# Kernel optimization log

Hardware: AMD Instinct MI355X
Metric: run time of the kernel (lower is better)

Reference implementation:

```python
import jax, jax.numpy as jnp
import numpy as np

B = 2048          # batch_size from init
D = 512           # embedding dim
TAU = 0.5         # temperature
EPS = 1e-12       # torch F.normalize eps


def _l2_normalize(x):
    n = jnp.linalg.norm(x, axis=1, keepdims=True)
    return x / jnp.maximum(n, EPS)


def setup_inputs() -> dict:
    key = jax.random.key(0)
    k1, k2 = jax.random.split(key)
    emb_i = jax.random.normal(k1, (2 * B, D), dtype=jnp.float32)
    emb_j = jax.random.normal(k2, (2 * B, D), dtype=jnp.float32)
    return {"emb_i": emb_i, "emb_j": emb_j}


def reference(emb_i, emb_j):
    z_i = _l2_normalize(emb_i)
    z_j = _l2_normalize(emb_j)
    rep = jnp.concatenate([z_i, z_j], axis=0)        # [4B, D], unit rows
    # cosine similarity of unit vectors == plain GEMM
    sim = rep @ rep.T                                # [4B, 4B]
    n = 4 * B
    pos1 = jnp.concatenate([jnp.diagonal(sim, B), jnp.diagonal(sim, -B)])        # [6B]
    pos2 = jnp.concatenate([jnp.diagonal(sim, 2 * B), jnp.diagonal(sim, -2 * B)])  # [4B]
    pos3 = jnp.concatenate([jnp.diagonal(sim, 3 * B), jnp.diagonal(sim, -3 * B)])  # [2B]
    nominator = (jnp.sum(jnp.exp(pos1 / TAU))
                 + jnp.sum(jnp.exp(pos2 / TAU))
                 + jnp.sum(jnp.exp(pos3 / TAU)))
    off_diag = 1.0 - jnp.eye(n, dtype=sim.dtype)
    denominator = jnp.sum(off_diag * jnp.exp(sim / TAU)) - nominator
    loss = -jnp.log(nominator / denominator) / (4 * B)
    return loss
```

## Files before the change

kernel.cpp:

```cpp
#include <hip/hip_runtime.h>
#include <stdint.h>

#define DIM       512
#define NROWS     8192
#define HALF_ROWS 4096
#define TILE      128
#define BK        32

typedef float  floatx4 __attribute__((ext_vector_type(4)));
typedef __bf16 bf16x8  __attribute__((ext_vector_type(8)));

__device__ __forceinline__ void async_copy16(const unsigned short* g, unsigned short* l) {
    __builtin_amdgcn_global_load_lds(
        (const __attribute__((address_space(1))) uint32_t*)(g),
        (__attribute__((address_space(3))) uint32_t*)(l),
        16, 0, 0);
}

__global__ void init_ws(double* ws) {
    ws[0] = 0.0;
    ws[1] = 0.0;
}

__global__ __launch_bounds__(256) void normalize_kernel(
    const float* __restrict__ emb_i, const float* __restrict__ emb_j,
    unsigned short* __restrict__ rep)
{
    const int wave = threadIdx.x >> 6;
    const int lane = threadIdx.x & 63;
    const int row  = blockIdx.x * 4 + wave;
    const float* src = (row < HALF_ROWS) ? (emb_i + (size_t)row * DIM)
                                         : (emb_j + (size_t)(row - HALF_ROWS) * DIM);
    const int c = lane * 8;
    float4 v0 = *(const float4*)(src + c);
    float4 v1 = *(const float4*)(src + c + 4);
    float s = v0.x*v0.x + v0.y*v0.y + v0.z*v0.z + v0.w*v0.w
            + v1.x*v1.x + v1.y*v1.y + v1.z*v1.z + v1.w*v1.w;
    #pragma unroll
    for (int off = 32; off; off >>= 1) s += __shfl_xor(s, off, 64);
    const float nrm = sqrtf(s);
    const float inv = 1.0f / fmaxf(nrm, 1e-12f);
    float f[8] = {v0.x*inv, v0.y*inv, v0.z*inv, v0.w*inv,
                  v1.x*inv, v1.y*inv, v1.z*inv, v1.w*inv};
    union { unsigned short h[8]; uint4 u; } pk;
    #pragma unroll
    for (int t = 0; t < 8; ++t) {
        uint32_t b = __float_as_uint(f[t]);
        b += 0x7FFFu + ((b >> 16) & 1u);
        pk.h[t] = (unsigned short)(b >> 16);
    }
    *(uint4*)(rep + (size_t)row * DIM + c) = pk.u;
}

__global__ __launch_bounds__(256) void gram_kernel(
    const unsigned short* __restrict__ rep, double* __restrict__ ws)
{
    const int bj = blockIdx.x, bi = blockIdx.y;
    if (bj < bi) return;

    __shared__ unsigned short As[TILE * BK];
    __shared__ unsigned short Bs[TILE * BK];
    __shared__ float red[8];

    const int tid  = threadIdx.x;
    const int wave = tid >> 6, lane = tid & 63;
    const int wm = wave >> 1, wn = wave & 1;
    const int m = lane & 15, quad = lane >> 4;

    floatx4 acc[4][4];
    #pragma unroll
    for (int a = 0; a < 4; ++a)
        #pragma unroll
        for (int b = 0; b < 4; ++b)
            #pragma unroll
            for (int e = 0; e < 4; ++e) acc[a][b][e] = 0.0f;

    const int i0 = bi * TILE, j0 = bj * TILE;

    for (int k0 = 0; k0 < DIM; k0 += BK) {
        #pragma unroll
        for (int r = 0; r < 2; ++r) {
            const int chunk = r * 256 + tid;
            const int row   = chunk >> 2;
            const int cc    = (chunk & 3) * 8;
            async_copy16(rep + (size_t)(i0 + row) * DIM + k0 + cc, As + chunk * 8);
            async_copy16(rep + (size_t)(j0 + row) * DIM + k0 + cc, Bs + chunk * 8);
        }
        __syncthreads();

        bf16x8 af[4], bfr[4];
        #pragma unroll
        for (int mt = 0; mt < 4; ++mt)
            af[mt] = *(const bf16x8*)(As + (wm * 64 + mt * 16 + m) * BK + quad * 8);
        #pragma unroll
        for (int nt = 0; nt < 4; ++nt)
            bfr[nt] = *(const bf16x8*)(Bs + (wn * 64 + nt * 16 + m) * BK + quad * 8);
        #pragma unroll
        for (int mt = 0; mt < 4; ++mt)
            #pragma unroll
            for (int nt = 0; nt < 4; ++nt)
                acc[mt][nt] = __builtin_amdgcn_mfma_f32_16x16x32_bf16(
                    af[mt], bfr[nt], acc[mt][nt], 0, 0, 0);
        __syncthreads();
    }

    float s_all = 0.0f, s_pos = 0.0f;
    const float LOG2E2 = 2.885390081777927f;
    #pragma unroll
    for (int mt = 0; mt < 4; ++mt) {
        const int ibase = i0 + wm * 64 + mt * 16 + quad * 4;
        #pragma unroll
        for (int nt = 0; nt < 4; ++nt) {
            const int j = j0 + wn * 64 + nt * 16 + m;
            const floatx4 a = acc[mt][nt];
            #pragma unroll
            for (int r2 = 0; r2 < 4; ++r2) {
                const int i = ibase + r2;
                const float e = exp2f(a[r2] * LOG2E2);
                if (i != j) s_all += e;
                const int d = j - i;
                if (d == 2048 || d == 4096 || d == 6144) s_pos += e;
            }
        }
    }
    #pragma unroll
    for (int off = 32; off; off >>= 1) {
        s_all += __shfl_xor(s_all, off, 64);
        s_pos += __shfl_xor(s_pos, off, 64);
    }
    if (lane == 0) { red[wave] = s_all; red[4 + wave] = s_pos; }
    __syncthreads();
    if (tid == 0) {
        const float w  = (bi == bj) ? 1.0f : 2.0f;
        const float ta = (red[0] + red[1] + red[2] + red[3]) * w;
        const float tp = (red[4] + red[5] + red[6] + red[7]) * w;
        atomicAdd(&ws[0], (double)ta);
        atomicAdd(&ws[1], (double)tp);
    }
}

__global__ void finalize_kernel(const double* __restrict__ ws, float* __restrict__ out) {
    const double nom = ws[1];
    const double den = ws[0] - nom;
    out[0] = (float)(-log(nom / den) / (double)NROWS);
}

extern "C" void kernel_launch(void* const* d_in, const int* in_sizes, int n_in,
                              void* d_out, int out_size, void* d_ws, size_t ws_size,
                              hipStream_t stream) {
    const float* emb_i = (const float*)d_in[0];
    const float* emb_j = (const float*)d_in[1];
    float* out = (float*)d_out;
    double* ws = (double*)d_ws;
    unsigned short* rep = (unsigned short*)((char*)d_ws + 256);

    hipLaunchKernelGGL(init_ws, dim3(1), dim3(1), 0, stream, ws);
    hipLaunchKernelGGL(normalize_kernel, dim3(NROWS / 4), dim3(256), 0, stream,
                       emb_i, emb_j, rep);
    hipLaunchKernelGGL(gram_kernel, dim3(64, 64), dim3(256), 0, stream, rep, ws);
    hipLaunchKernelGGL(finalize_kernel, dim3(1), dim3(1), 0, stream, ws, out);
}
```

Measured before the change: 147.8 us.

## Rewrite gram kernel as 256x256 triangular-tiled, swizzled, double-buffered MFMA pipeline

The gram kernel now uses 256x256 tiles with 8 waves. It launches only the 528 upper-triangle tiles instead of a 64x64 grid with early exits. K-slices of 64 are staged into XOR-swizzled LDS with asynchronous global-to-LDS copies, double-buffered and interleaved with MFMA phases under explicit barriers and priority hints. The init kernel is folded into the normalize kernel to save a launch. This is meant to raise MFMA utilisation and hide load latency, at the cost of more LDS (128KB per block), higher register pressure and a hand-tuned schedule that depends on vmcnt counts being exactly right.

New measurement: 136.4 us. 1.08x faster.

```diff
diff --git a/kernel.cpp b/kernel.cpp
--- a/kernel.cpp
+++ b/kernel.cpp
@@ -1,11 +1,12 @@
 #include <hip/hip_runtime.h>
 #include <stdint.h>
+#include <math.h>
 
 #define DIM       512
 #define NROWS     8192
 #define HALF_ROWS 4096
-#define TILE      128
-#define BK        32
+#define NT        32
+#define NTRI      528
 
 typedef float  floatx4 __attribute__((ext_vector_type(4)));
 typedef __bf16 bf16x8  __attribute__((ext_vector_type(8)));
@@ -17,15 +18,11 @@
         16, 0, 0);
 }
 
-__global__ void init_ws(double* ws) {
-    ws[0] = 0.0;
-    ws[1] = 0.0;
-}
-
 __global__ __launch_bounds__(256) void normalize_kernel(
     const float* __restrict__ emb_i, const float* __restrict__ emb_j,
-    unsigned short* __restrict__ rep)
+    unsigned short* __restrict__ rep, double* __restrict__ ws)
 {
+    if (blockIdx.x == 0 && threadIdx.x == 0) { ws[0] = 0.0; ws[1] = 0.0; }
     const int wave = threadIdx.x >> 6;
     const int lane = threadIdx.x & 63;
     const int row  = blockIdx.x * 4 + wave;
@@ -52,74 +49,155 @@
     *(uint4*)(rep + (size_t)row * DIM + c) = pk.u;
 }
 
-__global__ __launch_bounds__(256) void gram_kernel(
+__device__ __forceinline__ void stage_half(const unsigned short* __restrict__ rep,
+    int rowbase, int k0, unsigned short* lds, int tid)
+{
+    #pragma unroll
+    for (int l = 0; l < 2; ++l) {
+        const int ch  = l * 512 + tid;
+        const int row = ch >> 3;
+        const int s   = ch & 7;
+        const int col = (s ^ (row & 7)) << 3;
+        async_copy16(rep + (size_t)(rowbase + row) * DIM + (k0 + col), lds + ch * 8);
+    }
+}
+
+#define PH_BAR1() do { __builtin_amdgcn_s_barrier(); \
+    asm volatile("s_waitcnt lgkmcnt(0)" ::: "memory"); \
+    __builtin_amdgcn_sched_barrier(0); } while (0)
+
+#define PH_BAR2() do { __builtin_amdgcn_s_barrier(); \
+    __builtin_amdgcn_sched_barrier(0); } while (0)
+
+#define WAIT_VM(N) asm volatile("s_waitcnt vmcnt(" #N ")" ::: "memory")
+
+#define LOAD_A(BUF, MH) do { const unsigned short* Ah_ = sA[BUF][wm]; \
+    _Pragma("unroll") for (int mt = 0; mt < 4; ++mt) { \
+        const int r_ = (MH)*64 + mt*16 + m; \
+        a[mt][0] = *(const bf16x8*)((const char*)Ah_ + r_*128 + koff0); \
+        a[mt][1] = *(const bf16x8*)((const char*)Ah_ + r_*128 + koff1); } } while (0)
+
+#define LOAD_B(BUF, NS, DST) do { const unsigned short* Bh_ = sB[BUF][wn >> 1]; \
+    _Pragma("unroll") for (int nt = 0; nt < 2; ++nt) { \
+        const int r_ = (wn & 1)*64 + ((NS)*2 + nt)*16 + m; \
+        DST[nt][0] = *(const bf16x8*)((const char*)Bh_ + r_*128 + koff0); \
+        DST[nt][1] = *(const bf16x8*)((const char*)Bh_ + r_*128 + koff1); } } while (0)
+
+#define MFMA_Q(MH, NS, BB) do { \
+    __builtin_amdgcn_s_setprio(1); \
+    _Pragma("unroll") for (int mt = 0; mt < 4; ++mt) \
+      _Pragma("unroll") for (int nt = 0; nt < 2; ++nt) \
+        _Pragma("unroll") for (int kk = 0; kk < 2; ++kk) \
+          acc[(MH)*4 + mt][(NS)*2 + nt] = __builtin_amdgcn_mfma_f32_16x16x32_bf16( \
+              a[mt][kk], BB[nt][kk], acc[(MH)*4 + mt][(NS)*2 + nt], 0, 0, 0); \
+    __builtin_amdgcn_s_setprio(0); } while (0)
+
+__global__ __launch_bounds__(512, 2) void gram_kernel(
     const unsigned short* __restrict__ rep, double* __restrict__ ws)
 {
-    const int bj = blockIdx.x, bi = blockIdx.y;
-    if (bj < bi) return;
-
-    __shared__ unsigned short As[TILE * BK];
-    __shared__ unsigned short Bs[TILE * BK];
-    __shared__ float red[8];
+    __shared__ unsigned short sA[2][2][128 * 64];
+    __shared__ unsigned short sB[2][2][128 * 64];
+    __shared__ float red[16];
 
     const int tid  = threadIdx.x;
     const int wave = tid >> 6, lane = tid & 63;
-    const int wm = wave >> 1, wn = wave & 1;
+    const int wm = wave >> 2, wn = wave & 3;
     const int m = lane & 15, quad = lane >> 4;
-
-    floatx4 acc[4][4];
-    #pragma unroll
-    for (int a = 0; a < 4; ++a)
+    const int swz   = (m & 7) << 4;
+    const int koff0 = (0  + quad * 16) ^ swz;
+    const int koff1 = (64 + quad * 16) ^ swz;
+
+    const int u = blockIdx.x;
+    int bi = (int)((2.0f * NT + 1.0f
+                    - sqrtf((2.0f * NT + 1.0f) * (2.0f * NT + 1.0f) - 8.0f * (float)u)) * 0.5f);
+    while ((bi + 1) * NT - ((bi + 1) * bi) / 2 <= u) ++bi;
+    while (bi * NT - (bi * (bi - 1)) / 2 > u) --bi;
+    const int bj = bi + (u - (bi * NT - (bi * (bi - 1)) / 2));
+    const int i0 = bi * 256, j0 = bj * 256;
+
+    floatx4 acc[8][4];
+    #pragma unroll
+    for (int x = 0; x < 8; ++x)
         #pragma unroll
-        for (int b = 0; b < 4; ++b)
+        for (int y = 0; y < 4; ++y)
             #pragma unroll
-            for (int e = 0; e < 4; ++e) acc[a][b][e] = 0.0f;
-
-    const int i0 = bi * TILE, j0 = bj * TILE;
-
-    for (int k0 = 0; k0 < DIM; k0 += BK) {
-        #pragma unroll
-        for (int r = 0; r < 2; ++r) {
-            const int chunk = r * 256 + tid;
-            const int row   = chunk >> 2;
-            const int cc    = (chunk & 3) * 8;
-            async_copy16(rep + (size_t)(i0 + row) * DIM + k0 + cc, As + chunk * 8);
-            async_copy16(rep + (size_t)(j0 + row) * DIM + k0 + cc, Bs + chunk * 8);
-        }
-        __syncthreads();
-
-        bf16x8 af[4], bfr[4];
-        #pragma unroll
-        for (int mt = 0; mt < 4; ++mt)
-            af[mt] = *(const bf16x8*)(As + (wm * 64 + mt * 16 + m) * BK + quad * 8);
-        #pragma unroll
-        for (int nt = 0; nt < 4; ++nt)
-            bfr[nt] = *(const bf16x8*)(Bs + (wn * 64 + nt * 16 + m) * BK + quad * 8);
-        #pragma unroll
-        for (int mt = 0; mt < 4; ++mt)
-            #pragma unroll
-            for (int nt = 0; nt < 4; ++nt)
-                acc[mt][nt] = __builtin_amdgcn_mfma_f32_16x16x32_bf16(
-                    af[mt], bfr[nt], acc[mt][nt], 0, 0, 0);
-        __syncthreads();
-    }
+            for (int e = 0; e < 4; ++e) acc[x][y][e] = 0.0f;
+
+    bf16x8 a[4][2], bL[2][2], bR[2][2];
+
+    stage_half(rep, i0,       0,  sA[0][0], tid);
+    stage_half(rep, i0 + 128, 0,  sA[0][1], tid);
+    stage_half(rep, j0,       0,  sB[0][0], tid);
+    stage_half(rep, j0 + 128, 0,  sB[0][1], tid);
+    stage_half(rep, j0,       64, sB[1][0], tid);
+    stage_half(rep, j0 + 128, 64, sB[1][1], tid);
+    WAIT_VM(4);
+    __builtin_amdgcn_s_barrier();
+    __builtin_amdgcn_sched_barrier(0);
+
+    int kA1 = 64, kT2 = 128, kT3 = 192;
+    for (int it = 0; it < 3; ++it) {
+        LOAD_A(0, 0); LOAD_B(0, 0, bL);
+        stage_half(rep, i0, kA1, sA[1][0], tid);
+        PH_BAR1(); MFMA_Q(0, 0, bL); PH_BAR2();
+        LOAD_B(0, 1, bR);
+        stage_half(rep, i0 + 128, kA1, sA[1][1], tid);
+        PH_BAR1(); MFMA_Q(0, 1, bR); PH_BAR2();
+        LOAD_A(0, 1);
+        stage_half(rep, j0, kT2, sB[0][0], tid);
+        PH_BAR1(); MFMA_Q(1, 1, bR); PH_BAR2();
+        stage_half(rep, j0 + 128, kT2, sB[0][1], tid);
+        WAIT_VM(4);
+        PH_BAR1(); MFMA_Q(1, 0, bL); PH_BAR2();
+        LOAD_A(1, 0); LOAD_B(1, 0, bL);
+        stage_half(rep, i0, kT2, sA[0][0], tid);
+        PH_BAR1(); MFMA_Q(0, 0, bL); PH_BAR2();
+        LOAD_B(1, 1, bR);
+        stage_half(rep, i0 + 128, kT2, sA[0][1], tid);
+        PH_BAR1(); MFMA_Q(0, 1, bR); PH_BAR2();
+        LOAD_A(1, 1);
+        stage_half(rep, j0, kT3, sB[1][0], tid);
+        PH_BAR1(); MFMA_Q(1, 1, bR); PH_BAR2();
+        stage_half(rep, j0 + 128, kT3, sB[1][1], tid);
+        WAIT_VM(4);
+        PH_BAR1(); MFMA_Q(1, 0, bL); PH_BAR2();
+        kA1 += 128; kT2 += 128; kT3 += 128;
+    }
+
+    LOAD_A(0, 0); LOAD_B(0, 0, bL);
+    stage_half(rep, i0, 448, sA[1][0], tid);
+    PH_BAR1(); MFMA_Q(0, 0, bL); PH_BAR2();
+    LOAD_B(0, 1, bR);
+    stage_half(rep, i0 + 128, 448, sA[1][1], tid);
+    PH_BAR1(); MFMA_Q(0, 1, bR); PH_BAR2();
+    LOAD_A(0, 1);
+    PH_BAR1(); MFMA_Q(1, 1, bR); PH_BAR2();
+    WAIT_VM(0);
+    PH_BAR1(); MFMA_Q(1, 0, bL); PH_BAR2();
+    LOAD_A(1, 0); LOAD_B(1, 0, bL);
+    PH_BAR1(); MFMA_Q(0, 0, bL); PH_BAR2();
+    LOAD_B(1, 1, bR);
+    PH_BAR1(); MFMA_Q(0, 1, bR); PH_BAR2();
+    LOAD_A(1, 1);
+    PH_BAR1(); MFMA_Q(1, 1, bR); PH_BAR2();
+    MFMA_Q(1, 0, bL);
 
     float s_all = 0.0f, s_pos = 0.0f;
     const float LOG2E2 = 2.885390081777927f;
     #pragma unroll
-    for (int mt = 0; mt < 4; ++mt) {
-        const int ibase = i0 + wm * 64 + mt * 16 + quad * 4;
+    for (int mi = 0; mi < 8; ++mi) {
+        const int ibase = i0 + wm * 128 + mi * 16 + quad * 4;
         #pragma unroll
-        for (int nt = 0; nt < 4; ++nt) {
-            const int j = j0 + wn * 64 + nt * 16 + m;
-            const floatx4 a = acc[mt][nt];
+        for (int nj = 0; nj < 4; ++nj) {
+            const int j = j0 + wn * 64 + nj * 16 + m;
+            const floatx4 v = acc[mi][nj];
             #pragma unroll
-            for (int r2 = 0; r2 < 4; ++r2) {
-                const int i = ibase + r2;
-                const float e = exp2f(a[r2] * LOG2E2);
-                if (i != j) s_all += e;
+            for (int e = 0; e < 4; ++e) {
+                const int i = ibase + e;
+                const float ex = exp2f(v[e] * LOG2E2);
+                if (i != j) s_all += ex;
                 const int d = j - i;
-                if (d == 2048 || d == 4096 || d == 6144) s_pos += e;
+                if (d == 2048 || d == 4096 || d == 6144) s_pos += ex;
             }
         }
     }
@@ -128,14 +206,15 @@
         s_all += __shfl_xor(s_all, off, 64);
         s_pos += __shfl_xor(s_pos, off, 64);
     }
-    if (lane == 0) { red[wave] = s_all; red[4 + wave] = s_pos; }
+    if (lane == 0) { red[wave] = s_all; red[8 + wave] = s_pos; }
     __syncthreads();
     if (tid == 0) {
-        const float w  = (bi == bj) ? 1.0f : 2.0f;
-        const float ta = (red[0] + red[1] + red[2] + red[3]) * w;
-        const float tp = (red[4] + red[5] + red[6] + red[7]) * w;
-        atomicAdd(&ws[0], (double)ta);
-        atomicAdd(&ws[1], (double)tp);
+        float ta = 0.0f, tp = 0.0f;
+        #pragma unroll
+        for (int w2 = 0; w2 < 8; ++w2) { ta += red[w2]; tp += red[8 + w2]; }
+        const float wgt = (bi == bj) ? 1.0f : 2.0f;
+        atomicAdd(&ws[0], (double)(ta * wgt));
+        atomicAdd(&ws[1], (double)(tp * wgt));
     }
 }
 
@@ -154,9 +233,8 @@
     double* ws = (double*)d_ws;
     unsigned short* rep = (unsigned short*)((char*)d_ws + 256);
 
-    hipLaunchKernelGGL(init_ws, dim3(1), dim3(1), 0, stream, ws);
     hipLaunchKernelGGL(normalize_kernel, dim3(NROWS / 4), dim3(256), 0, stream,
-                       emb_i, emb_j, rep);
-    hipLaunchKernelGGL(gram_kernel, dim3(64, 64), dim3(256), 0, stream, rep, ws);
+                       emb_i, emb_j, rep, ws);
+    hipLaunchKernelGGL(gram_kernel, dim3(NTRI), dim3(512), 0, stream, rep, ws);
     hipLaunchKernelGGL(finalize_kernel, dim3(1), dim3(1), 0, stream, ws, out);
 }
```
